# Kernel optimization log

Hardware: AMD Instinct MI355X
Metric: run time of the kernel (lower is better)

Reference implementation:

```python
import jax, jax.numpy as jnp
import numpy as np

B = 131072      # batch
IN = 1024       # input_dim
H = 384         # hidden[0]
L = 128         # latent_dim = hidden[1]
K = 32          # slots_k
R = 2           # top_r
TAU = 0.7


def setup_inputs() -> dict:
    key = jax.random.key(0)
    ks = jax.random.split(key, 8)
    s = 0.02
    f32 = jnp.float32
    return {
        "x":  jax.random.normal(ks[0], (B, IN), f32),
        "w1": jax.random.normal(ks[1], (IN, H), f32) * s,
        "b1": jnp.zeros((H,), f32),
        "w2": jax.random.normal(ks[2], (H, L), f32) * s,
        "b2": jnp.zeros((L,), f32),
        "mk": jax.random.normal(ks[3], (K, L), f32) * s,  # memory_keys
        "mv": jax.random.normal(ks[4], (K, L), f32) * s,  # memory_values
        "w3": jax.random.normal(ks[5], (2 * L, H), f32) * s,
        "b3": jnp.zeros((H,), f32),
        "w4": jax.random.normal(ks[6], (H, 1), f32) * s,
        "b4": jnp.zeros((1,), f32),
    }


def reference(x, w1, b1, w2, b2, mk, mv, w3, b3, w4, b4):
    # block_a: Linear -> GELU -> (Dropout=id in eval) -> Linear -> GELU
    z = jax.nn.gelu(x @ w1 + b1, approximate=False)
    z = jax.nn.gelu(z @ w2 + b2, approximate=False)          # [B, L]

    # top-r slot attention over memory bank
    logits = (z @ mk.T) / TAU                                 # [B, K]
    _, idx = jax.lax.top_k(logits, R)                         # [B, R]
    keep = jax.nn.one_hot(idx, K, dtype=logits.dtype).sum(-2) > 0  # [B, K] bool
    masked = jnp.where(keep, logits, -jnp.inf)
    attn = jax.nn.softmax(masked, axis=-1)                    # [B, K]
    mem = attn @ mv                                           # [B, L]

    fused = jnp.concatenate([z, mem], axis=-1)                # [B, 2L]

    # default head: Linear -> GELU -> Linear(.,1)
    h = jax.nn.gelu(fused @ w3 + b3, approximate=False)
    logit = (h @ w4 + b4)[..., 0]                             # [B]
    return jax.nn.sigmoid(logit)
```

## Files before the change

### kernel.cpp

```cpp
#include <hip/hip_runtime.h>

#define BATCH   131072
#define INDIM   1024
#define BM      64
#define BDIM    512
#define NBLK    (BATCH / BM)

#define WT_OFF   0
#define XT0_OFF  49152
#define XT1_OFF  57344
#define Z1_OFF   0
#define W2T0_OFF 50176
#define W2T1_OFF 58368
#define FZ_OFF   0
#define RP_OFF   33792
#define W3T_OFF  42240
#define CB_OFF   66816
#define B1S_OFF  (CB_OFF)
#define B2S_OFF  (CB_OFF + 1536)
#define B3S_OFF  (CB_OFF + 2048)
#define W4S_OFF  (CB_OFF + 3584)
#define MKS_OFF  (CB_OFF + 5120)
#define SMEM_BYTES (CB_OFF + 13824)

typedef unsigned short u16;
typedef u16    u16x8  __attribute__((ext_vector_type(8)));
typedef u16    u16x4  __attribute__((ext_vector_type(4)));
typedef __bf16 bf16x8 __attribute__((ext_vector_type(8)));
typedef __bf16 bf16x4 __attribute__((ext_vector_type(4)));
typedef float  f32x4  __attribute__((ext_vector_type(4)));

__device__ __forceinline__ u16 f2bf(float f) {
  unsigned u = __float_as_uint(f);
  u += 0x7FFFu + ((u >> 16) & 1u);
  return (u16)(u >> 16);
}

__device__ __forceinline__ float gelu_fast(float v) {
  float t = v * v;
  float u = v * fmaf(t, 0.0356774081f, 0.7978845608f);
  float e = __builtin_amdgcn_exp2f(u * -2.885390082f);
  return v * __builtin_amdgcn_rcpf(1.0f + e);
}

__device__ __forceinline__ f32x4 mfma16(u16x8 a, u16x8 b, f32x4 c) {
  return __builtin_amdgcn_mfma_f32_16x16x32_bf16(
      __builtin_bit_cast(bf16x8, a), __builtin_bit_cast(bf16x8, b), c, 0, 0, 0);
}

__device__ __forceinline__ u16x8 cvt8(float4 a, float4 b) {
  bf16x8 r;
  r[0]=(__bf16)a.x; r[1]=(__bf16)a.y; r[2]=(__bf16)a.z; r[3]=(__bf16)a.w;
  r[4]=(__bf16)b.x; r[5]=(__bf16)b.y; r[6]=(__bf16)b.z; r[7]=(__bf16)b.w;
  return __builtin_bit_cast(u16x8, r);
}
__device__ __forceinline__ u16x4 cvt4(float4 a) {
  bf16x4 r;
  r[0]=(__bf16)a.x; r[1]=(__bf16)a.y; r[2]=(__bf16)a.z; r[3]=(__bf16)a.w;
  return __builtin_bit_cast(u16x4, r);
}

typedef __attribute__((address_space(3))) unsigned int       lds_u32;
typedef __attribute__((address_space(1))) const unsigned int glb_u32;
__device__ __forceinline__ void gload16(const void* g, void* l) {
  __builtin_amdgcn_global_load_lds((glb_u32*)g, (lds_u32*)l, 16, 0, 0);
}

#define FENCE_SCHED __builtin_amdgcn_sched_barrier(0)
#define WAIT_LGKM0 do { asm volatile("s_waitcnt lgkmcnt(0)" ::: "memory"); FENCE_SCHED; } while (0)
#define WAIT_VMN(N) do { asm volatile("s_waitcnt vmcnt(" #N ")" ::: "memory"); FENCE_SCHED; } while (0)
#define BARRIER_LGKM do { \
  asm volatile("s_waitcnt lgkmcnt(0)" ::: "memory"); \
  __builtin_amdgcn_s_barrier(); FENCE_SCHED; } while (0)

__global__ void prep_kernel(const float* __restrict__ w1, const float* __restrict__ w2,
                            const float* __restrict__ w3, u16* __restrict__ w1s,
                            u16* __restrict__ w2s, u16* __restrict__ w3s) {
  int i = blockIdx.x * 256 + threadIdx.x;
  if (i < 393216) {
    int t = i / 24576, p = i % 24576;
    int r = p >> 6, q = p & 63, cp = q >> 3, o = q & 7;
    int k = t * 64 + ((cp ^ (r & 7)) << 3) + o;
    w1s[i] = f2bf(w1[k * 384 + r]);
  } else if (i < 442368) {
    int j = i - 393216;
    int t = j / 4096, p = j % 4096;
    int r = p >> 5, q = p & 31, cp = q >> 3, o = q & 7;
    int k = t * 32 + ((cp ^ ((r >> 1) & 3)) << 3) + o;
    w2s[j] = f2bf(w2[k * 128 + r]);
  } else if (i < 540672) {
    int j = i - 442368;
    int t = j / 12288, p = j % 12288;
    int r = p >> 5, q = p & 31, cp = q >> 3, o = q & 7;
    int k = t * 32 + ((cp ^ ((r >> 1) & 3)) << 3) + o;
    w3s[j] = f2bf(w3[k * 384 + r]);
  }
}

__global__ __launch_bounds__(BDIM, 4) void fused_kernel(
    const float* __restrict__ x,  const u16* __restrict__ w1s,
    const float* __restrict__ b1, const u16* __restrict__ w2s,
    const float* __restrict__ b2, const float* __restrict__ mkw,
    const float* __restrict__ mvw, const u16* __restrict__ w3s,
    const float* __restrict__ b3, const float* __restrict__ w4,
    const float* __restrict__ b4, float* __restrict__ out) {
  extern __shared__ char smem[];
  u16*   z1  = (u16*)(smem + Z1_OFF);
  u16*   fz  = (u16*)(smem + FZ_OFF);
  u16*   w3t = (u16*)(smem + W3T_OFF);
  float* b1s = (float*)(smem + B1S_OFF);
  float* b2s = (float*)(smem + B2S_OFF);
  float* b3s = (float*)(smem + B3S_OFF);
  float* w4s = (float*)(smem + W4S_OFF);
  u16*   mks = (u16*)(smem + MKS_OFF);
  float* rowpart = (float*)(smem + RP_OFF);

  const int tid  = threadIdx.x;
  const int lane = tid & 63;
  const int wid  = tid >> 6;
  const int l15  = lane & 15;
  const int g    = lane >> 4;
  const int swz8 = l15 & 7;
  const int swz4 = (l15 >> 1) & 3;
  const int row0 = blockIdx.x * BM;
  const int wrow = wid * 48;
  const int wstrip = wid * 3072;

  {
    const u16* ws = w1s + wstrip + lane * 8;
    u16* wd = (u16*)(smem + WT_OFF) + wstrip;
    #pragma unroll
    for (int i = 0; i < 6; ++i) gload16(ws + i * 512, wd + i * 512);
  }
  FENCE_SCHED;
  const int xrow = tid >> 3, xoct = tid & 7;
  const float* xp = x + (long)(row0 + xrow) * INDIM + xoct * 8;
  const int xdst = xrow * 64 + ((xoct ^ (xrow & 7)) << 3);
  float4 xa = *(const float4*)xp, xb = *(const float4*)(xp + 4);

  if (tid < 384) b1s[tid] = b1[tid];
  if (tid < 128) b2s[tid] = b2[tid];
  if (tid < 384) b3s[tid] = b3[tid];
  if (tid < 384) w4s[tid] = w4[tid];
  {
    int r = tid >> 4, cc = (tid & 15) * 8;
    const float4* p = (const float4*)(mkw + r * 128 + cc);
    *(u16x8*)(mks + r * 136 + cc) = cvt8(p[0], p[1]);
  }
  *(u16x8*)((u16*)(smem + XT0_OFF) + xdst) = cvt8(xa, xb);
  { const float* p = xp + 64; xa = *(const float4*)p; xb = *(const float4*)(p + 4); }
  BARRIER_LGKM;

  f32x4 acc[4][3];
  #pragma unroll
  for (int m = 0; m < 4; ++m)
    #pragma unroll
    for (int n = 0; n < 3; ++n) acc[m][n] = (f32x4){0.f, 0.f, 0.f, 0.f};

  const u16* wtb = (const u16*)(smem + WT_OFF);
  for (int kt = 0; kt < 16; ++kt) {
    if (kt < 15) { WAIT_VMN(2); } else { WAIT_VMN(0); }
    const u16* xtb = (const u16*)(smem + ((kt & 1) ? XT1_OFF : XT0_OFF));
    u16x8 af[4], bfr[3];
    const int c0 = (g ^ swz8) * 8;
    #pragma unroll
    for (int m = 0; m < 4; ++m) af[m] = *(const u16x8*)(xtb + (m * 16 + l15) * 64 + c0);
    #pragma unroll
    for (int n = 0; n < 3; ++n) bfr[n] = *(const u16x8*)(wtb + (wrow + n * 16 + l15) * 64 + c0);
    #pragma unroll
    for (int m = 0; m < 4; ++m)
      #pragma unroll
      for (int n = 0; n < 3; ++n) acc[m][n] = mfma16(bfr[n], af[m], acc[m][n]);
    const int c1 = ((g + 4) ^ swz8) * 8;
    #pragma unroll
    for (int m = 0; m < 4; ++m) af[m] = *(const u16x8*)(xtb + (m * 16 + l15) * 64 + c1);
    #pragma unroll
    for (int n = 0; n < 3; ++n) bfr[n] = *(const u16x8*)(wtb + (wrow + n * 16 + l15) * 64 + c1);
    WAIT_LGKM0;
    if (kt < 15) {
      const u16* ws = w1s + (kt + 1) * 24576 + wstrip + lane * 8;
      u16* wd = (u16*)(smem + WT_OFF) + wstrip;
      #pragma unroll
      for (int i = 0; i < 6; ++i) gload16(ws + i * 512, wd + i * 512);
      FENCE_SCHED;
      u16* xn = (u16*)(smem + ((kt & 1) ? XT0_OFF : XT1_OFF));
      *(u16x8*)(xn + xdst) = cvt8(xa, xb);
      if (kt < 14) {
        const float* p = xp + (kt + 2) * 64;
        xa = *(const float4*)p; xb = *(const float4*)(p + 4);
      }
      BARRIER_LGKM;
    }
    #pragma unroll
    for (int m = 0; m < 4; ++m)
      #pragma unroll
      for (int n = 0; n < 3; ++n) acc[m][n] = mfma16(bfr[n], af[m], acc[m][n]);
  }
  BARRIER_LGKM;

  {
    const u16* s2 = w2s + wid * 512 + lane * 8;
    gload16(s2, (u16*)(smem + W2T0_OFF) + wid * 512);
    const u16* s2b = w2s + 4096 + wid * 512 + lane * 8;
    gload16(s2b, (u16*)(smem + W2T1_OFF) + wid * 512);
  }
  #pragma unroll
  for (int m = 0; m < 4; ++m) {
    #pragma unroll
    for (int n = 0; n < 3; ++n) {
      int col = wrow + n * 16 + g * 4;
      float4 bv = *(const float4*)(b1s + col);
      f32x4 a = acc[m][n];
      float4 gv = {gelu_fast(a[0] + bv.x), gelu_fast(a[1] + bv.y),
                   gelu_fast(a[2] + bv.z), gelu_fast(a[3] + bv.w)};
      *(u16x4*)(z1 + (m * 16 + l15) * 392 + col) = cvt4(gv);
    }
  }
  BARRIER_LGKM;

  f32x4 acc2[4];
  #pragma unroll
  for (int m = 0; m < 4; ++m) acc2[m] = (f32x4){0.f, 0.f, 0.f, 0.f};
  for (int kt = 0; kt < 12; ++kt) {
    if (kt < 10) { WAIT_VMN(1); } else { WAIT_VMN(0); }
    const u16* wb = (const u16*)(smem + ((kt & 1) ? W2T1_OFF : W2T0_OFF));
    u16x8 a2f[4];
    #pragma unroll
    for (int m = 0; m < 4; ++m)
      a2f[m] = *(const u16x8*)(z1 + (m * 16 + l15) * 392 + kt * 32 + g * 8);
    u16x8 b2f = *(const u16x8*)(wb + (wid * 16 + l15) * 32 + (g ^ swz4) * 8);
    WAIT_LGKM0;
    if (kt < 10) {
      const u16* s2 = w2s + (kt + 2) * 4096 + wid * 512 + lane * 8;
      gload16(s2, (u16*)(smem + ((kt & 1) ? W2T1_OFF : W2T0_OFF)) + wid * 512);
    }
    #pragma unroll
    for (int m = 0; m < 4; ++m) acc2[m] = mfma16(b2f, a2f[m], acc2[m]);
  }
  BARRIER_LGKM;

  {
    const u16* s3 = w3s + wid * 1536 + lane * 8;
    u16* d3 = w3t + wid * 1536;
    gload16(s3, d3); gload16(s3 + 512, d3 + 512); gload16(s3 + 1024, d3 + 1024);
  }
  #pragma unroll
  for (int m = 0; m < 4; ++m) {
    int col = wid * 16 + g * 4;
    float4 bv = *(const float4*)(b2s + col);
    f32x4 a = acc2[m];
    float4 gv = {gelu_fast(a[0] + bv.x), gelu_fast(a[1] + bv.y),
                 gelu_fast(a[2] + bv.z), gelu_fast(a[3] + bv.w)};
    *(u16x4*)(fz + (m * 16 + l15) * 264 + col) = cvt4(gv);
  }
  BARRIER_LGKM;

  if (wid < 4) {
    const int wr = wid * 16 + l15;
    f32x4 accl[2] = {(f32x4){0,0,0,0}, (f32x4){0,0,0,0}};
    #pragma unroll
    for (int ks = 0; ks < 4; ++ks) {
      u16x8 afz = *(const u16x8*)(fz + wr * 264 + ks * 32 + g * 8);
      u16x8 k0  = *(const u16x8*)(mks + l15 * 136 + ks * 32 + g * 8);
      u16x8 k1  = *(const u16x8*)(mks + (16 + l15) * 136 + ks * 32 + g * 8);
      accl[0] = mfma16(k0, afz, accl[0]);
      accl[1] = mfma16(k1, afz, accl[1]);
    }
    float m1 = -3.4e38f, m2 = -3.4e38f; int i1 = -1, i2 = -1;
    #pragma unroll
    for (int n = 0; n < 2; ++n)
      #pragma unroll
      for (int j = 0; j < 4; ++j) {
        float v = accl[n][j]; int idx = n * 16 + g * 4 + j;
        if (v > m1) { m2 = m1; i2 = i1; m1 = v; i1 = idx; }
        else if (v > m2) { m2 = v; i2 = idx; }
      }
    #pragma unroll
    for (int d = 16; d <= 32; d <<= 1) {
      float om1 = __shfl_xor(m1, d); int oi1 = __shfl_xor(i1, d);
      float om2 = __shfl_xor(m2, d); int oi2 = __shfl_xor(i2, d);
      bool take = (om1 > m1) || (om1 == m1 && oi1 < i1);
      if (take) {
        float nm2; int ni2;
        if (m1 > om2 || (m1 == om2 && i1 < oi2)) { nm2 = m1; ni2 = i1; }
        else { nm2 = om2; ni2 = oi2; }
        m1 = om1; i1 = oi1; m2 = nm2; i2 = ni2;
      } else {
        if (om1 > m2 || (om1 == m2 && oi1 < i2)) { m2 = om1; i2 = oi1; }
      }
    }
    float a1 = __builtin_amdgcn_rcpf(
        1.0f + __builtin_amdgcn_exp2f((m2 - m1) * (1.44269504f / 0.7f)));
    float a2 = 1.0f - a1;
    const float* v1 = mvw + i1 * 128 + g * 32;
    const float* v2 = mvw + i2 * 128 + g * 32;
    #pragma unroll
    for (int c = 0; c < 4; ++c) {
      float4 A0 = *(const float4*)(v1 + c * 8), A1 = *(const float4*)(v1 + c * 8 + 4);
      float4 B0 = *(const float4*)(v2 + c * 8), B1 = *(const float4*)(v2 + c * 8 + 4);
      float4 r0 = {a1*A0.x + a2*B0.x, a1*A0.y + a2*B0.y, a1*A0.z + a2*B0.z, a1*A0.w + a2*B0.w};
      float4 r1 = {a1*A1.x + a2*B1.x, a1*A1.y + a2*B1.y, a1*A1.z + a2*B1.z, a1*A1.w + a2*B1.w};
      *(u16x8*)(fz + wr * 264 + 128 + g * 32 + c * 8) = cvt8(r0, r1);
    }
  }
  BARRIER_LGKM;

  f32x4 acc3[4][3];
  #pragma unroll
  for (int m = 0; m < 4; ++m)
    #pragma unroll
    for (int n = 0; n < 3; ++n) acc3[m][n] = (f32x4){0.f, 0.f, 0.f, 0.f};
  for (int kt = 0; kt < 8; ++kt) {
    WAIT_VMN(0);
    u16x8 a3f[4], b3f[3];
    #pragma unroll
    for (int m = 0; m < 4; ++m)
      a3f[m] = *(const u16x8*)(fz + (m * 16 + l15) * 264 + kt * 32 + g * 8);
    #pragma unroll
    for (int n = 0; n < 3; ++n)
      b3f[n] = *(const u16x8*)(w3t + (wrow + n * 16 + l15) * 32 + (g ^ swz4) * 8);
    WAIT_LGKM0;
    if (kt < 7) {
      const u16* s3 = w3s + (kt + 1) * 12288 + wid * 1536 + lane * 8;
      u16* d3 = w3t + wid * 1536;
      gload16(s3, d3); gload16(s3 + 512, d3 + 512); gload16(s3 + 1024, d3 + 1024);
    }
    #pragma unroll
    for (int m = 0; m < 4; ++m)
      #pragma unroll
      for (int n = 0; n < 3; ++n) acc3[m][n] = mfma16(b3f[n], a3f[m], acc3[m][n]);
  }

  #pragma unroll
  for (int m = 0; m < 4; ++m) {
    float s = 0.f;
    #pragma unroll
    for (int n = 0; n < 3; ++n) {
      int col = wrow + n * 16 + g * 4;
      float4 bv = *(const float4*)(b3s + col);
      float4 wv = *(const float4*)(w4s + col);
      f32x4 a = acc3[m][n];
      s += gelu_fast(a[0] + bv.x) * wv.x + gelu_fast(a[1] + bv.y) * wv.y +
           gelu_fast(a[2] + bv.z) * wv.z + gelu_fast(a[3] + bv.w) * wv.w;
    }
    s += __shfl_xor(s, 16);
    s += __shfl_xor(s, 32);
    if (lane < 16) rowpart[(m * 16 + l15) * 8 + wid] = s;
  }
  BARRIER_LGKM;
  if (tid < BM) {
    const float4* rp = (const float4*)(rowpart + tid * 8);
    float4 p0 = rp[0], p1 = rp[1];
    float lg = b4[0] + p0.x + p0.y + p0.z + p0.w + p1.x + p1.y + p1.z + p1.w;
    out[row0 + tid] = __builtin_amdgcn_rcpf(1.0f + __builtin_amdgcn_exp2f(-lg * 1.44269504f));
  }
}

extern "C" void kernel_launch(void* const* d_in, const int* in_sizes, int n_in,
                              void* d_out, int out_size, void* d_ws, size_t ws_size,
                              hipStream_t stream) {
  const float* x  = (const float*)d_in[0];
  const float* w1 = (const float*)d_in[1];
  const float* b1 = (const float*)d_in[2];
  const float* w2 = (const float*)d_in[3];
  const float* b2 = (const float*)d_in[4];
  const float* mk = (const float*)d_in[5];
  const float* mv = (const float*)d_in[6];
  const float* w3 = (const float*)d_in[7];
  const float* b3 = (const float*)d_in[8];
  const float* w4 = (const float*)d_in[9];
  const float* b4 = (const float*)d_in[10];

  u16* w1s = (u16*)d_ws;
  u16* w2s = w1s + 393216;
  u16* w3s = w1s + 442368;

  prep_kernel<<<2112, 256, 0, stream>>>(w1, w2, w3, w1s, w2s, w3s);

  (void)hipFuncSetAttribute(reinterpret_cast<const void*>(fused_kernel),
                            hipFuncAttributeMaxDynamicSharedMemorySize, SMEM_BYTES);
  fused_kernel<<<NBLK, BDIM, SMEM_BYTES, stream>>>(x, w1s, b1, w2s, b2, mk, mv, w3s,
                                                   b3, w4, b4, (float*)d_out);
}
```

Baseline: 232.0 us.

## Double-buffer W1 tiles with k=32 sub-tiles to overlap loads with MFMA

Restructures the first GEMM's K loop from a single 64-wide W1 buffer, refilled after all its fragments were read, into two 32-wide W1 buffers (wt0/wt1). Each half-tile's refill is issued right after its fragments are read, so global-to-LDS loads overlap MFMA work on the other buffer. X staging is split into two 32-wide halves per step, with one barrier per 64 of K and an explicit prologue and epilogue. The prep kernel re-swizzles W1 to the k=32 layout, and the swizzle index is unified across stages. It adds code size and register pressure and relies on exact vmcnt bookkeeping.

```diff
diff --git a/kernel.cpp b/kernel.cpp
--- a/kernel.cpp
+++ b/kernel.cpp
@@ -6,9 +6,10 @@
 #define BDIM    512
 #define NBLK    (BATCH / BM)
 
-#define WT_OFF   0
-#define XT0_OFF  49152
-#define XT1_OFF  57344
+#define WT0_OFF  0
+#define WT1_OFF  24576
+#define XTA_OFF  49152
+#define XTB_OFF  57344
 #define Z1_OFF   0
 #define W2T0_OFF 50176
 #define W2T1_OFF 58368
@@ -78,9 +79,9 @@
                             u16* __restrict__ w2s, u16* __restrict__ w3s) {
   int i = blockIdx.x * 256 + threadIdx.x;
   if (i < 393216) {
-    int t = i / 24576, p = i % 24576;
-    int r = p >> 6, q = p & 63, cp = q >> 3, o = q & 7;
-    int k = t * 64 + ((cp ^ (r & 7)) << 3) + o;
+    int t = i / 12288, p = i % 12288;
+    int r = p >> 5, q = p & 31, cp = q >> 3, o = q & 7;
+    int k = t * 32 + ((cp ^ ((r >> 1) & 3)) << 3) + o;
     w1s[i] = f2bf(w1[k * 384 + r]);
   } else if (i < 442368) {
     int j = i - 393216;
@@ -108,6 +109,8 @@
   u16*   z1  = (u16*)(smem + Z1_OFF);
   u16*   fz  = (u16*)(smem + FZ_OFF);
   u16*   w3t = (u16*)(smem + W3T_OFF);
+  u16*   wt0 = (u16*)(smem + WT0_OFF);
+  u16*   wt1 = (u16*)(smem + WT1_OFF);
   float* b1s = (float*)(smem + B1S_OFF);
   float* b2s = (float*)(smem + B2S_OFF);
   float* b3s = (float*)(smem + B3S_OFF);
@@ -120,23 +123,10 @@
   const int wid  = tid >> 6;
   const int l15  = lane & 15;
   const int g    = lane >> 4;
-  const int swz8 = l15 & 7;
-  const int swz4 = (l15 >> 1) & 3;
+  const int sw8  = (g ^ ((l15 >> 1) & 3)) * 8;
   const int row0 = blockIdx.x * BM;
   const int wrow = wid * 48;
-  const int wstrip = wid * 3072;
-
-  {
-    const u16* ws = w1s + wstrip + lane * 8;
-    u16* wd = (u16*)(smem + WT_OFF) + wstrip;
-    #pragma unroll
-    for (int i = 0; i < 6; ++i) gload16(ws + i * 512, wd + i * 512);
-  }
-  FENCE_SCHED;
-  const int xrow = tid >> 3, xoct = tid & 7;
-  const float* xp = x + (long)(row0 + xrow) * INDIM + xoct * 8;
-  const int xdst = xrow * 64 + ((xoct ^ (xrow & 7)) << 3);
-  float4 xa = *(const float4*)xp, xb = *(const float4*)(xp + 4);
+  const int wstrip = wid * 1536;
 
   if (tid < 384) b1s[tid] = b1[tid];
   if (tid < 128) b2s[tid] = b2[tid];
@@ -147,8 +137,22 @@
     const float4* p = (const float4*)(mkw + r * 128 + cc);
     *(u16x8*)(mks + r * 136 + cc) = cvt8(p[0], p[1]);
   }
-  *(u16x8*)((u16*)(smem + XT0_OFF) + xdst) = cvt8(xa, xb);
-  { const float* p = xp + 64; xa = *(const float4*)p; xb = *(const float4*)(p + 4); }
+  {
+    const u16* ws = w1s + wstrip + lane * 8;
+    gload16(ws, wt0 + wstrip); gload16(ws + 512, wt0 + wstrip + 512);
+    gload16(ws + 1024, wt0 + wstrip + 1024);
+    const u16* ws1 = ws + 12288;
+    gload16(ws1, wt1 + wstrip); gload16(ws1 + 512, wt1 + wstrip + 512);
+    gload16(ws1 + 1024, wt1 + wstrip + 1024);
+  }
+  FENCE_SCHED;
+  const int xrow = tid >> 3, xq = tid & 7;
+  const float* xp = x + (long)(row0 + xrow) * INDIM + xq * 4;
+  const int xpub = xrow * 32 + (((xq >> 1) ^ ((xrow >> 1) & 3)) << 3) + (xq & 1) * 4;
+  float4 xA = *(const float4*)xp, xB = *(const float4*)(xp + 32);
+  *(u16x4*)((u16*)(smem + XTA_OFF) + xpub)        = cvt4(xA);
+  *(u16x4*)((u16*)(smem + XTA_OFF) + 2048 + xpub) = cvt4(xB);
+  xA = *(const float4*)(xp + 64); xB = *(const float4*)(xp + 96);
   BARRIER_LGKM;
 
   f32x4 acc[4][3];
@@ -157,44 +161,114 @@
     #pragma unroll
     for (int n = 0; n < 3; ++n) acc[m][n] = (f32x4){0.f, 0.f, 0.f, 0.f};
 
-  const u16* wtb = (const u16*)(smem + WT_OFF);
-  for (int kt = 0; kt < 16; ++kt) {
-    if (kt < 15) { WAIT_VMN(2); } else { WAIT_VMN(0); }
-    const u16* xtb = (const u16*)(smem + ((kt & 1) ? XT1_OFF : XT0_OFF));
-    u16x8 af[4], bfr[3];
-    const int c0 = (g ^ swz8) * 8;
-    #pragma unroll
-    for (int m = 0; m < 4; ++m) af[m] = *(const u16x8*)(xtb + (m * 16 + l15) * 64 + c0);
-    #pragma unroll
-    for (int n = 0; n < 3; ++n) bfr[n] = *(const u16x8*)(wtb + (wrow + n * 16 + l15) * 64 + c0);
-    #pragma unroll
-    for (int m = 0; m < 4; ++m)
-      #pragma unroll
-      for (int n = 0; n < 3; ++n) acc[m][n] = mfma16(bfr[n], af[m], acc[m][n]);
-    const int c1 = ((g + 4) ^ swz8) * 8;
-    #pragma unroll
-    for (int m = 0; m < 4; ++m) af[m] = *(const u16x8*)(xtb + (m * 16 + l15) * 64 + c1);
-    #pragma unroll
-    for (int n = 0; n < 3; ++n) bfr[n] = *(const u16x8*)(wtb + (wrow + n * 16 + l15) * 64 + c1);
-    WAIT_LGKM0;
-    if (kt < 15) {
-      const u16* ws = w1s + (kt + 1) * 24576 + wstrip + lane * 8;
-      u16* wd = (u16*)(smem + WT_OFF) + wstrip;
-      #pragma unroll
-      for (int i = 0; i < 6; ++i) gload16(ws + i * 512, wd + i * 512);
-      FENCE_SCHED;
-      u16* xn = (u16*)(smem + ((kt & 1) ? XT0_OFF : XT1_OFF));
-      *(u16x8*)(xn + xdst) = cvt8(xa, xb);
-      if (kt < 14) {
-        const float* p = xp + (kt + 2) * 64;
-        xa = *(const float4*)p; xb = *(const float4*)(p + 4);
-      }
-      BARRIER_LGKM;
-    }
-    #pragma unroll
-    for (int m = 0; m < 4; ++m)
-      #pragma unroll
-      for (int n = 0; n < 3; ++n) acc[m][n] = mfma16(bfr[n], af[m], acc[m][n]);
+  for (int p = 0; p < 14; ++p) {
+    const u16* xrb = (const u16*)(smem + ((p & 1) ? XTB_OFF : XTA_OFF));
+    u16* xwb = (u16*)(smem + ((p & 1) ? XTA_OFF : XTB_OFF));
+    WAIT_VMN(5);
+    {
+      u16x8 af[4], bfr[3];
+      #pragma unroll
+      for (int m = 0; m < 4; ++m) af[m] = *(const u16x8*)(xrb + (m * 16 + l15) * 32 + sw8);
+      #pragma unroll
+      for (int n = 0; n < 3; ++n) bfr[n] = *(const u16x8*)(wt0 + (wrow + n * 16 + l15) * 32 + sw8);
+      WAIT_LGKM0;
+      const u16* ws = w1s + (2 * p + 2) * 12288 + wstrip + lane * 8;
+      gload16(ws, wt0 + wstrip); gload16(ws + 512, wt0 + wstrip + 512);
+      gload16(ws + 1024, wt0 + wstrip + 1024);
+      #pragma unroll
+      for (int m = 0; m < 4; ++m)
+        #pragma unroll
+        for (int n = 0; n < 3; ++n) acc[m][n] = mfma16(bfr[n], af[m], acc[m][n]);
+    }
+    WAIT_VMN(5);
+    {
+      u16x8 af[4], bfr[3];
+      #pragma unroll
+      for (int m = 0; m < 4; ++m) af[m] = *(const u16x8*)(xrb + 2048 + (m * 16 + l15) * 32 + sw8);
+      #pragma unroll
+      for (int n = 0; n < 3; ++n) bfr[n] = *(const u16x8*)(wt1 + (wrow + n * 16 + l15) * 32 + sw8);
+      WAIT_LGKM0;
+      const u16* ws = w1s + (2 * p + 3) * 12288 + wstrip + lane * 8;
+      gload16(ws, wt1 + wstrip); gload16(ws + 512, wt1 + wstrip + 512);
+      gload16(ws + 1024, wt1 + wstrip + 1024);
+      #pragma unroll
+      for (int m = 0; m < 4; ++m)
+        #pragma unroll
+        for (int n = 0; n < 3; ++n) acc[m][n] = mfma16(bfr[n], af[m], acc[m][n]);
+    }
+    *(u16x4*)(xwb + xpub)        = cvt4(xA);
+    *(u16x4*)(xwb + 2048 + xpub) = cvt4(xB);
+    xA = *(const float4*)(xp + (2 * p + 4) * 32);
+    xB = *(const float4*)(xp + (2 * p + 5) * 32);
+    BARRIER_LGKM;
+  }
+  {
+    const u16* xrb = (const u16*)(smem + XTA_OFF);
+    u16* xwb = (u16*)(smem + XTB_OFF);
+    WAIT_VMN(5);
+    {
+      u16x8 af[4], bfr[3];
+      #pragma unroll
+      for (int m = 0; m < 4; ++m) af[m] = *(const u16x8*)(xrb + (m * 16 + l15) * 32 + sw8);
+      #pragma unroll
+      for (int n = 0; n < 3; ++n) bfr[n] = *(const u16x8*)(wt0 + (wrow + n * 16 + l15) * 32 + sw8);
+      WAIT_LGKM0;
+      const u16* ws = w1s + 30 * 12288 + wstrip + lane * 8;
+      gload16(ws, wt0 + wstrip); gload16(ws + 512, wt0 + wstrip + 512);
+      gload16(ws + 1024, wt0 + wstrip + 1024);
+      #pragma unroll
+      for (int m = 0; m < 4; ++m)
+        #pragma unroll
+        for (int n = 0; n < 3; ++n) acc[m][n] = mfma16(bfr[n], af[m], acc[m][n]);
+    }
+    WAIT_VMN(5);
+    {
+      u16x8 af[4], bfr[3];
+      #pragma unroll
+      for (int m = 0; m < 4; ++m) af[m] = *(const u16x8*)(xrb + 2048 + (m * 16 + l15) * 32 + sw8);
+      #pragma unroll
+      for (int n = 0; n < 3; ++n) bfr[n] = *(const u16x8*)(wt1 + (wrow + n * 16 + l15) * 32 + sw8);
+      WAIT_LGKM0;
+      const u16* ws = w1s + 31 * 12288 + wstrip + lane * 8;
+      gload16(ws, wt1 + wstrip); gload16(ws + 512, wt1 + wstrip + 512);
+      gload16(ws + 1024, wt1 + wstrip + 1024);
+      #pragma unroll
+      for (int m = 0; m < 4; ++m)
+        #pragma unroll
+        for (int n = 0; n < 3; ++n) acc[m][n] = mfma16(bfr[n], af[m], acc[m][n]);
+    }
+    *(u16x4*)(xwb + xpub)        = cvt4(xA);
+    *(u16x4*)(xwb + 2048 + xpub) = cvt4(xB);
+    BARRIER_LGKM;
+  }
+  {
+    const u16* xrb = (const u16*)(smem + XTB_OFF);
+    WAIT_VMN(3);
+    {
+      u16x8 af[4], bfr[3];
+      #pragma unroll
+      for (int m = 0; m < 4; ++m) af[m] = *(const u16x8*)(xrb + (m * 16 + l15) * 32 + sw8);
+      #pragma unroll
+      for (int n = 0; n < 3; ++n) bfr[n] = *(const u16x8*)(wt0 + (wrow + n * 16 + l15) * 32 + sw8);
+      WAIT_LGKM0;
+      #pragma unroll
+      for (int m = 0; m < 4; ++m)
+        #pragma unroll
+        for (int n = 0; n < 3; ++n) acc[m][n] = mfma16(bfr[n], af[m], acc[m][n]);
+    }
+    WAIT_VMN(0);
+    {
+      u16x8 af[4], bfr[3];
+      #pragma unroll
+      for (int m = 0; m < 4; ++m) af[m] = *(const u16x8*)(xrb + 2048 + (m * 16 + l15) * 32 + sw8);
+      #pragma unroll
+      for (int n = 0; n < 3; ++n) bfr[n] = *(const u16x8*)(wt1 + (wrow + n * 16 + l15) * 32 + sw8);
+      WAIT_LGKM0;
+      #pragma unroll
+      for (int m = 0; m < 4; ++m)
+        #pragma unroll
+        for (int n = 0; n < 3; ++n) acc[m][n] = mfma16(bfr[n], af[m], acc[m][n]);
+    }
   }
   BARRIER_LGKM;
 
@@ -228,7 +302,7 @@
     #pragma unroll
     for (int m = 0; m < 4; ++m)
       a2f[m] = *(const u16x8*)(z1 + (m * 16 + l15) * 392 + kt * 32 + g * 8);
-    u16x8 b2f = *(const u16x8*)(wb + (wid * 16 + l15) * 32 + (g ^ swz4) * 8);
+    u16x8 b2f = *(const u16x8*)(wb + (wid * 16 + l15) * 32 + sw8);
     WAIT_LGKM0;
     if (kt < 10) {
       const u16* s2 = w2s + (kt + 2) * 4096 + wid * 512 + lane * 8;
@@ -318,7 +392,7 @@
       a3f[m] = *(const u16x8*)(fz + (m * 16 + l15) * 264 + kt * 32 + g * 8);
     #pragma unroll
     for (int n = 0; n < 3; ++n)
-      b3f[n] = *(const u16x8*)(w3t + (wrow + n * 16 + l15) * 32 + (g ^ swz4) * 8);
+      b3f[n] = *(const u16x8*)(w3t + (wrow + n * 16 + l15) * 32 + sw8);
     WAIT_LGKM0;
     if (kt < 7) {
       const u16* s3 = w3s + (kt + 1) * 12288 + wid * 1536 + lane * 8;
```

After: 229.0 us. No clear change (-1.3%).

## Load weights directly into registers in MFMA fragment layout instead of staging via LDS

Applied to the files above, without the earlier changes.

The prep kernel now lays out W1, W2 and W3 in per-lane MFMA fragment order, so each wave reads its weight fragments straight from global/L2 into registers with register double-buffering. The LDS weight staging (global_load_lds, swizzles, vmcnt waits) is removed, leaving LDS for the x tiles and the activations. The x tile is restructured into two 32-wide K halves per barrier step, which halves the number of block barriers in the first GEMM. Launch bounds drop to 2 blocks per CU, which gives more registers but lowers occupancy, and every block now re-reads the weights from L2 with no reuse in LDS.

```diff
diff --git a/kernel.cpp b/kernel.cpp
--- a/kernel.cpp
+++ b/kernel.cpp
@@ -6,16 +6,12 @@
 #define BDIM    512
 #define NBLK    (BATCH / BM)
 
-#define WT_OFF   0
-#define XT0_OFF  49152
-#define XT1_OFF  57344
 #define Z1_OFF   0
-#define W2T0_OFF 50176
-#define W2T1_OFF 58368
 #define FZ_OFF   0
 #define RP_OFF   33792
-#define W3T_OFF  42240
-#define CB_OFF   66816
+#define XTA_OFF  50176
+#define XTB_OFF  58368
+#define CB_OFF   66560
 #define B1S_OFF  (CB_OFF)
 #define B2S_OFF  (CB_OFF + 1536)
 #define B3S_OFF  (CB_OFF + 2048)
@@ -60,54 +56,53 @@
   return __builtin_bit_cast(u16x4, r);
 }
 
-typedef __attribute__((address_space(3))) unsigned int       lds_u32;
-typedef __attribute__((address_space(1))) const unsigned int glb_u32;
-__device__ __forceinline__ void gload16(const void* g, void* l) {
-  __builtin_amdgcn_global_load_lds((glb_u32*)g, (lds_u32*)l, 16, 0, 0);
-}
-
-#define FENCE_SCHED __builtin_amdgcn_sched_barrier(0)
-#define WAIT_LGKM0 do { asm volatile("s_waitcnt lgkmcnt(0)" ::: "memory"); FENCE_SCHED; } while (0)
-#define WAIT_VMN(N) do { asm volatile("s_waitcnt vmcnt(" #N ")" ::: "memory"); FENCE_SCHED; } while (0)
 #define BARRIER_LGKM do { \
   asm volatile("s_waitcnt lgkmcnt(0)" ::: "memory"); \
-  __builtin_amdgcn_s_barrier(); FENCE_SCHED; } while (0)
+  __builtin_amdgcn_s_barrier(); \
+  __builtin_amdgcn_sched_barrier(0); } while (0)
 
 __global__ void prep_kernel(const float* __restrict__ w1, const float* __restrict__ w2,
-                            const float* __restrict__ w3, u16* __restrict__ w1s,
-                            u16* __restrict__ w2s, u16* __restrict__ w3s) {
+                            const float* __restrict__ w3, u16* __restrict__ w1f,
+                            u16* __restrict__ w2f, u16* __restrict__ w3f) {
   int i = blockIdx.x * 256 + threadIdx.x;
   if (i < 393216) {
-    int t = i / 24576, p = i % 24576;
-    int r = p >> 6, q = p & 63, cp = q >> 3, o = q & 7;
-    int k = t * 64 + ((cp ^ (r & 7)) << 3) + o;
-    w1s[i] = f2bf(w1[k * 384 + r]);
+    int o = i & 7, lane = (i >> 3) & 63;
+    int rest = i >> 9;
+    int n = rest % 3, rw = rest / 3;
+    int wid = rw & 7, kt = rw >> 3;
+    int col = wid * 48 + n * 16 + (lane & 15);
+    int k = kt * 32 + (lane >> 4) * 8 + o;
+    w1f[i] = f2bf(w1[k * 384 + col]);
   } else if (i < 442368) {
     int j = i - 393216;
-    int t = j / 4096, p = j % 4096;
-    int r = p >> 5, q = p & 31, cp = q >> 3, o = q & 7;
-    int k = t * 32 + ((cp ^ ((r >> 1) & 3)) << 3) + o;
-    w2s[j] = f2bf(w2[k * 128 + r]);
+    int o = j & 7, lane = (j >> 3) & 63;
+    int rest = j >> 9;
+    int wid = rest & 7, kt = rest >> 3;
+    int col = wid * 16 + (lane & 15);
+    int k = kt * 32 + (lane >> 4) * 8 + o;
+    w2f[j] = f2bf(w2[k * 128 + col]);
   } else if (i < 540672) {
     int j = i - 442368;
-    int t = j / 12288, p = j % 12288;
-    int r = p >> 5, q = p & 31, cp = q >> 3, o = q & 7;
-    int k = t * 32 + ((cp ^ ((r >> 1) & 3)) << 3) + o;
-    w3s[j] = f2bf(w3[k * 384 + r]);
-  }
-}
-
-__global__ __launch_bounds__(BDIM, 4) void fused_kernel(
-    const float* __restrict__ x,  const u16* __restrict__ w1s,
-    const float* __restrict__ b1, const u16* __restrict__ w2s,
+    int o = j & 7, lane = (j >> 3) & 63;
+    int rest = j >> 9;
+    int n = rest % 3, rw = rest / 3;
+    int wid = rw & 7, kt = rw >> 3;
+    int col = wid * 48 + n * 16 + (lane & 15);
+    int k = kt * 32 + (lane >> 4) * 8 + o;
+    w3f[j] = f2bf(w3[k * 384 + col]);
+  }
+}
+
+__global__ __launch_bounds__(BDIM, 2) void fused_kernel(
+    const float* __restrict__ x,  const u16* __restrict__ w1f,
+    const float* __restrict__ b1, const u16* __restrict__ w2f,
     const float* __restrict__ b2, const float* __restrict__ mkw,
-    const float* __restrict__ mvw, const u16* __restrict__ w3s,
+    const float* __restrict__ mvw, const u16* __restrict__ w3f,
     const float* __restrict__ b3, const float* __restrict__ w4,
     const float* __restrict__ b4, float* __restrict__ out) {
   extern __shared__ char smem[];
   u16*   z1  = (u16*)(smem + Z1_OFF);
   u16*   fz  = (u16*)(smem + FZ_OFF);
-  u16*   w3t = (u16*)(smem + W3T_OFF);
   float* b1s = (float*)(smem + B1S_OFF);
   float* b2s = (float*)(smem + B2S_OFF);
   float* b3s = (float*)(smem + B3S_OFF);
@@ -120,23 +115,22 @@
   const int wid  = tid >> 6;
   const int l15  = lane & 15;
   const int g    = lane >> 4;
-  const int swz8 = l15 & 7;
-  const int swz4 = (l15 >> 1) & 3;
+  const int sw8  = (g ^ ((l15 >> 1) & 3)) * 8;
   const int row0 = blockIdx.x * BM;
   const int wrow = wid * 48;
-  const int wstrip = wid * 3072;
-
-  {
-    const u16* ws = w1s + wstrip + lane * 8;
-    u16* wd = (u16*)(smem + WT_OFF) + wstrip;
-    #pragma unroll
-    for (int i = 0; i < 6; ++i) gload16(ws + i * 512, wd + i * 512);
-  }
-  FENCE_SCHED;
-  const int xrow = tid >> 3, xoct = tid & 7;
-  const float* xp = x + (long)(row0 + xrow) * INDIM + xoct * 8;
-  const int xdst = xrow * 64 + ((xoct ^ (xrow & 7)) << 3);
-  float4 xa = *(const float4*)xp, xb = *(const float4*)(xp + 4);
+
+  const u16* wp1 = w1f + wid * 1536 + lane * 8;
+  u16x8 wf0[3], wf1[3];
+  #pragma unroll
+  for (int n = 0; n < 3; ++n) wf0[n] = *(const u16x8*)(wp1 + n * 512);
+  #pragma unroll
+  for (int n = 0; n < 3; ++n) wf1[n] = *(const u16x8*)(wp1 + 12288 + n * 512);
+
+  const int xrow = tid >> 3, xq = tid & 7;
+  const float* xp = x + (long)(row0 + xrow) * INDIM + xq * 4;
+  const int xpub = xrow * 32 + (((xq >> 1) ^ ((xrow >> 1) & 3)) << 3) + (xq & 1) * 4;
+  float4 xA = *(const float4*)xp;
+  float4 xB = *(const float4*)(xp + 32);
 
   if (tid < 384) b1s[tid] = b1[tid];
   if (tid < 128) b2s[tid] = b2[tid];
@@ -144,11 +138,12 @@
   if (tid < 384) w4s[tid] = w4[tid];
   {
     int r = tid >> 4, cc = (tid & 15) * 8;
-    const float4* p = (const float4*)(mkw + r * 128 + cc);
-    *(u16x8*)(mks + r * 136 + cc) = cvt8(p[0], p[1]);
-  }
-  *(u16x8*)((u16*)(smem + XT0_OFF) + xdst) = cvt8(xa, xb);
-  { const float* p = xp + 64; xa = *(const float4*)p; xb = *(const float4*)(p + 4); }
+    const float4* pm = (const float4*)(mkw + r * 128 + cc);
+    *(u16x8*)(mks + r * 136 + cc) = cvt8(pm[0], pm[1]);
+  }
+  *(u16x4*)((u16*)(smem + XTA_OFF) + xpub)        = cvt4(xA);
+  *(u16x4*)((u16*)(smem + XTA_OFF) + 2048 + xpub) = cvt4(xB);
+  xA = *(const float4*)(xp + 64); xB = *(const float4*)(xp + 96);
   BARRIER_LGKM;
 
   f32x4 acc[4][3];
@@ -157,52 +152,52 @@
     #pragma unroll
     for (int n = 0; n < 3; ++n) acc[m][n] = (f32x4){0.f, 0.f, 0.f, 0.f};
 
-  const u16* wtb = (const u16*)(smem + WT_OFF);
-  for (int kt = 0; kt < 16; ++kt) {
-    if (kt < 15) { WAIT_VMN(2); } else { WAIT_VMN(0); }
-    const u16* xtb = (const u16*)(smem + ((kt & 1) ? XT1_OFF : XT0_OFF));
-    u16x8 af[4], bfr[3];
-    const int c0 = (g ^ swz8) * 8;
-    #pragma unroll
-    for (int m = 0; m < 4; ++m) af[m] = *(const u16x8*)(xtb + (m * 16 + l15) * 64 + c0);
-    #pragma unroll
-    for (int n = 0; n < 3; ++n) bfr[n] = *(const u16x8*)(wtb + (wrow + n * 16 + l15) * 64 + c0);
-    #pragma unroll
-    for (int m = 0; m < 4; ++m)
-      #pragma unroll
-      for (int n = 0; n < 3; ++n) acc[m][n] = mfma16(bfr[n], af[m], acc[m][n]);
-    const int c1 = ((g + 4) ^ swz8) * 8;
-    #pragma unroll
-    for (int m = 0; m < 4; ++m) af[m] = *(const u16x8*)(xtb + (m * 16 + l15) * 64 + c1);
-    #pragma unroll
-    for (int n = 0; n < 3; ++n) bfr[n] = *(const u16x8*)(wtb + (wrow + n * 16 + l15) * 64 + c1);
-    WAIT_LGKM0;
-    if (kt < 15) {
-      const u16* ws = w1s + (kt + 1) * 24576 + wstrip + lane * 8;
-      u16* wd = (u16*)(smem + WT_OFF) + wstrip;
-      #pragma unroll
-      for (int i = 0; i < 6; ++i) gload16(ws + i * 512, wd + i * 512);
-      FENCE_SCHED;
-      u16* xn = (u16*)(smem + ((kt & 1) ? XT0_OFF : XT1_OFF));
-      *(u16x8*)(xn + xdst) = cvt8(xa, xb);
-      if (kt < 14) {
-        const float* p = xp + (kt + 2) * 64;
-        xa = *(const float4*)p; xb = *(const float4*)(p + 4);
-      }
-      BARRIER_LGKM;
-    }
-    #pragma unroll
-    for (int m = 0; m < 4; ++m)
-      #pragma unroll
-      for (int n = 0; n < 3; ++n) acc[m][n] = mfma16(bfr[n], af[m], acc[m][n]);
-  }
-  BARRIER_LGKM;
-
+  for (int p = 0; p < 15; ++p) {
+    const u16* xrb = (const u16*)(smem + ((p & 1) ? XTB_OFF : XTA_OFF));
+    u16* xwb = (u16*)(smem + ((p & 1) ? XTA_OFF : XTB_OFF));
+    u16x8 af0[4], af1[4];
+    #pragma unroll
+    for (int m = 0; m < 4; ++m) af0[m] = *(const u16x8*)(xrb + (m * 16 + l15) * 32 + sw8);
+    #pragma unroll
+    for (int m = 0; m < 4; ++m) af1[m] = *(const u16x8*)(xrb + 2048 + (m * 16 + l15) * 32 + sw8);
+    u16x8 wn0[3], wn1[3];
+    #pragma unroll
+    for (int n = 0; n < 3; ++n) wn0[n] = *(const u16x8*)(wp1 + (2 * p + 2) * 12288 + n * 512);
+    #pragma unroll
+    for (int n = 0; n < 3; ++n) wn1[n] = *(const u16x8*)(wp1 + (2 * p + 3) * 12288 + n * 512);
+    #pragma unroll
+    for (int m = 0; m < 4; ++m)
+      #pragma unroll
+      for (int n = 0; n < 3; ++n) acc[m][n] = mfma16(wf0[n], af0[m], acc[m][n]);
+    *(u16x4*)(xwb + xpub)        = cvt4(xA);
+    *(u16x4*)(xwb + 2048 + xpub) = cvt4(xB);
+    if (p < 14) {
+      xA = *(const float4*)(xp + (2 * p + 4) * 32);
+      xB = *(const float4*)(xp + (2 * p + 5) * 32);
+    }
+    #pragma unroll
+    for (int m = 0; m < 4; ++m)
+      #pragma unroll
+      for (int n = 0; n < 3; ++n) acc[m][n] = mfma16(wf1[n], af1[m], acc[m][n]);
+    #pragma unroll
+    for (int n = 0; n < 3; ++n) { wf0[n] = wn0[n]; wf1[n] = wn1[n]; }
+    BARRIER_LGKM;
+  }
   {
-    const u16* s2 = w2s + wid * 512 + lane * 8;
-    gload16(s2, (u16*)(smem + W2T0_OFF) + wid * 512);
-    const u16* s2b = w2s + 4096 + wid * 512 + lane * 8;
-    gload16(s2b, (u16*)(smem + W2T1_OFF) + wid * 512);
+    const u16* xrb = (const u16*)(smem + XTB_OFF);
+    u16x8 af0[4], af1[4];
+    #pragma unroll
+    for (int m = 0; m < 4; ++m) af0[m] = *(const u16x8*)(xrb + (m * 16 + l15) * 32 + sw8);
+    #pragma unroll
+    for (int m = 0; m < 4; ++m) af1[m] = *(const u16x8*)(xrb + 2048 + (m * 16 + l15) * 32 + sw8);
+    #pragma unroll
+    for (int m = 0; m < 4; ++m)
+      #pragma unroll
+      for (int n = 0; n < 3; ++n) acc[m][n] = mfma16(wf0[n], af0[m], acc[m][n]);
+    #pragma unroll
+    for (int m = 0; m < 4; ++m)
+      #pragma unroll
+      for (int n = 0; n < 3; ++n) acc[m][n] = mfma16(wf1[n], af1[m], acc[m][n]);
   }
   #pragma unroll
   for (int m = 0; m < 4; ++m) {
@@ -218,32 +213,23 @@
   }
   BARRIER_LGKM;
 
+  const u16* wp2 = w2f + wid * 512 + lane * 8;
   f32x4 acc2[4];
   #pragma unroll
   for (int m = 0; m < 4; ++m) acc2[m] = (f32x4){0.f, 0.f, 0.f, 0.f};
+  u16x8 w2c = *(const u16x8*)wp2;
   for (int kt = 0; kt < 12; ++kt) {
-    if (kt < 10) { WAIT_VMN(1); } else { WAIT_VMN(0); }
-    const u16* wb = (const u16*)(smem + ((kt & 1) ? W2T1_OFF : W2T0_OFF));
     u16x8 a2f[4];
     #pragma unroll
     for (int m = 0; m < 4; ++m)
       a2f[m] = *(const u16x8*)(z1 + (m * 16 + l15) * 392 + kt * 32 + g * 8);
-    u16x8 b2f = *(const u16x8*)(wb + (wid * 16 + l15) * 32 + (g ^ swz4) * 8);
-    WAIT_LGKM0;
-    if (kt < 10) {
-      const u16* s2 = w2s + (kt + 2) * 4096 + wid * 512 + lane * 8;
-      gload16(s2, (u16*)(smem + ((kt & 1) ? W2T1_OFF : W2T0_OFF)) + wid * 512);
-    }
-    #pragma unroll
-    for (int m = 0; m < 4; ++m) acc2[m] = mfma16(b2f, a2f[m], acc2[m]);
-  }
-  BARRIER_LGKM;
-
-  {
-    const u16* s3 = w3s + wid * 1536 + lane * 8;
-    u16* d3 = w3t + wid * 1536;
-    gload16(s3, d3); gload16(s3 + 512, d3 + 512); gload16(s3 + 1024, d3 + 1024);
-  }
+    u16x8 w2n = (kt < 11) ? *(const u16x8*)(wp2 + (kt + 1) * 4096) : w2c;
+    #pragma unroll
+    for (int m = 0; m < 4; ++m) acc2[m] = mfma16(w2c, a2f[m], acc2[m]);
+    w2c = w2n;
+  }
+  BARRIER_LGKM;
+
   #pragma unroll
   for (int m = 0; m < 4; ++m) {
     int col = wid * 16 + g * 4;
@@ -305,30 +291,29 @@
   }
   BARRIER_LGKM;
 
+  const u16* wp3 = w3f + wid * 1536 + lane * 8;
   f32x4 acc3[4][3];
   #pragma unroll
   for (int m = 0; m < 4; ++m)
     #pragma unroll
     for (int n = 0; n < 3; ++n) acc3[m][n] = (f32x4){0.f, 0.f, 0.f, 0.f};
+  u16x8 w3c[3];
+  #pragma unroll
+  for (int n = 0; n < 3; ++n) w3c[n] = *(const u16x8*)(wp3 + n * 512);
   for (int kt = 0; kt < 8; ++kt) {
-    WAIT_VMN(0);
-    u16x8 a3f[4], b3f[3];
+    u16x8 a3f[4], w3n[3];
     #pragma unroll
     for (int m = 0; m < 4; ++m)
       a3f[m] = *(const u16x8*)(fz + (m * 16 + l15) * 264 + kt * 32 + g * 8);
     #pragma unroll
     for (int n = 0; n < 3; ++n)
-      b3f[n] = *(const u16x8*)(w3t + (wrow + n * 16 + l15) * 32 + (g ^ swz4) * 8);
-    WAIT_LGKM0;
-    if (kt < 7) {
-      const u16* s3 = w3s + (kt + 1) * 12288 + wid * 1536 + lane * 8;
-      u16* d3 = w3t + wid * 1536;
-      gload16(s3, d3); gload16(s3 + 512, d3 + 512); gload16(s3 + 1024, d3 + 1024);
-    }
-    #pragma unroll
-    for (int m = 0; m < 4; ++m)
-      #pragma unroll
-      for (int n = 0; n < 3; ++n) acc3[m][n] = mfma16(b3f[n], a3f[m], acc3[m][n]);
+      w3n[n] = (kt < 7) ? *(const u16x8*)(wp3 + (kt + 1) * 12288 + n * 512) : w3c[n];
+    #pragma unroll
+    for (int m = 0; m < 4; ++m)
+      #pragma unroll
+      for (int n = 0; n < 3; ++n) acc3[m][n] = mfma16(w3c[n], a3f[m], acc3[m][n]);
+    #pragma unroll
+    for (int n = 0; n < 3; ++n) w3c[n] = w3n[n];
   }
 
   #pragma unroll
@@ -371,14 +356,14 @@
   const float* w4 = (const float*)d_in[9];
   const float* b4 = (const float*)d_in[10];
 
-  u16* w1s = (u16*)d_ws;
-  u16* w2s = w1s + 393216;
-  u16* w3s = w1s + 442368;
-
-  prep_kernel<<<2112, 256, 0, stream>>>(w1, w2, w3, w1s, w2s, w3s);
+  u16* w1f = (u16*)d_ws;
+  u16* w2f = w1f + 393216;
+  u16* w3f = w1f + 442368;
+
+  prep_kernel<<<2112, 256, 0, stream>>>(w1, w2, w3, w1f, w2f, w3f);
 
   (void)hipFuncSetAttribute(reinterpret_cast<const void*>(fused_kernel),
                             hipFuncAttributeMaxDynamicSharedMemorySize, SMEM_BYTES);
-  fused_kernel<<<NBLK, BDIM, SMEM_BYTES, stream>>>(x, w1s, b1, w2s, b2, mk, mv, w3s,
+  fused_kernel<<<NBLK, BDIM, SMEM_BYTES, stream>>>(x, w1f, b1, w2f, b2, mk, mv, w3f,
                                                    b3, w4, b4, (float*)d_out);
 }
```

Measured after the change: 271.8 us. +17.2%, slower.

## Double-buffer W1 tiles with K=32 steps and register-prefetched fragments in GEMM1

Applied to the files above, without the earlier changes.

Restructures the first GEMM's main loop from 16 steps of K=64 with a single W1 buffer into 32 steps of K=32. W1 and X each get two LDS buffers, the W1 prep layout and swizzle change to match, and the next step's fragments are loaded into registers while the current MFMAs run. MFMA sections are wrapped in s_setprio in GEMM1 and GEMM3. Launch bounds drop from 4 to 2 blocks per SM, which loosens register pressure but may lower occupancy, and the loop now takes twice as many barriers.

```diff
diff --git a/kernel.cpp b/kernel.cpp
--- a/kernel.cpp
+++ b/kernel.cpp
@@ -6,9 +6,10 @@
 #define BDIM    512
 #define NBLK    (BATCH / BM)
 
-#define WT_OFF   0
+#define WT0_OFF  0
+#define WT1_OFF  24576
 #define XT0_OFF  49152
-#define XT1_OFF  57344
+#define XT1_OFF  53248
 #define Z1_OFF   0
 #define W2T0_OFF 50176
 #define W2T1_OFF 58368
@@ -69,6 +70,7 @@
 #define FENCE_SCHED __builtin_amdgcn_sched_barrier(0)
 #define WAIT_LGKM0 do { asm volatile("s_waitcnt lgkmcnt(0)" ::: "memory"); FENCE_SCHED; } while (0)
 #define WAIT_VMN(N) do { asm volatile("s_waitcnt vmcnt(" #N ")" ::: "memory"); FENCE_SCHED; } while (0)
+#define SOFT_VM0 asm volatile("s_waitcnt vmcnt(0)" ::: "memory")
 #define BARRIER_LGKM do { \
   asm volatile("s_waitcnt lgkmcnt(0)" ::: "memory"); \
   __builtin_amdgcn_s_barrier(); FENCE_SCHED; } while (0)
@@ -78,9 +80,9 @@
                             u16* __restrict__ w2s, u16* __restrict__ w3s) {
   int i = blockIdx.x * 256 + threadIdx.x;
   if (i < 393216) {
-    int t = i / 24576, p = i % 24576;
-    int r = p >> 6, q = p & 63, cp = q >> 3, o = q & 7;
-    int k = t * 64 + ((cp ^ (r & 7)) << 3) + o;
+    int t = i / 12288, p = i % 12288;
+    int r = p >> 5, q = p & 31, cp = q >> 3, o = q & 7;
+    int k = t * 32 + ((cp ^ ((r >> 1) & 3)) << 3) + o;
     w1s[i] = f2bf(w1[k * 384 + r]);
   } else if (i < 442368) {
     int j = i - 393216;
@@ -97,7 +99,7 @@
   }
 }
 
-__global__ __launch_bounds__(BDIM, 4) void fused_kernel(
+__global__ __launch_bounds__(BDIM, 2) void fused_kernel(
     const float* __restrict__ x,  const u16* __restrict__ w1s,
     const float* __restrict__ b1, const u16* __restrict__ w2s,
     const float* __restrict__ b2, const float* __restrict__ mkw,
@@ -108,6 +110,8 @@
   u16*   z1  = (u16*)(smem + Z1_OFF);
   u16*   fz  = (u16*)(smem + FZ_OFF);
   u16*   w3t = (u16*)(smem + W3T_OFF);
+  u16*   wt0 = (u16*)(smem + WT0_OFF);
+  u16*   wt1 = (u16*)(smem + WT1_OFF);
   float* b1s = (float*)(smem + B1S_OFF);
   float* b2s = (float*)(smem + B2S_OFF);
   float* b3s = (float*)(smem + B3S_OFF);
@@ -120,23 +124,10 @@
   const int wid  = tid >> 6;
   const int l15  = lane & 15;
   const int g    = lane >> 4;
-  const int swz8 = l15 & 7;
-  const int swz4 = (l15 >> 1) & 3;
+  const int sw8  = (g ^ ((l15 >> 1) & 3)) * 8;
   const int row0 = blockIdx.x * BM;
   const int wrow = wid * 48;
-  const int wstrip = wid * 3072;
-
-  {
-    const u16* ws = w1s + wstrip + lane * 8;
-    u16* wd = (u16*)(smem + WT_OFF) + wstrip;
-    #pragma unroll
-    for (int i = 0; i < 6; ++i) gload16(ws + i * 512, wd + i * 512);
-  }
-  FENCE_SCHED;
-  const int xrow = tid >> 3, xoct = tid & 7;
-  const float* xp = x + (long)(row0 + xrow) * INDIM + xoct * 8;
-  const int xdst = xrow * 64 + ((xoct ^ (xrow & 7)) << 3);
-  float4 xa = *(const float4*)xp, xb = *(const float4*)(xp + 4);
+  const int wstrip = wid * 1536;
 
   if (tid < 384) b1s[tid] = b1[tid];
   if (tid < 128) b2s[tid] = b2[tid];
@@ -144,11 +135,26 @@
   if (tid < 384) w4s[tid] = w4[tid];
   {
     int r = tid >> 4, cc = (tid & 15) * 8;
-    const float4* p = (const float4*)(mkw + r * 128 + cc);
-    *(u16x8*)(mks + r * 136 + cc) = cvt8(p[0], p[1]);
-  }
-  *(u16x8*)((u16*)(smem + XT0_OFF) + xdst) = cvt8(xa, xb);
-  { const float* p = xp + 64; xa = *(const float4*)p; xb = *(const float4*)(p + 4); }
+    const float4* pm = (const float4*)(mkw + r * 128 + cc);
+    *(u16x8*)(mks + r * 136 + cc) = cvt8(pm[0], pm[1]);
+  }
+  {
+    const u16* ws = w1s + wstrip + lane * 8;
+    gload16(ws, wt0 + wstrip); gload16(ws + 512, wt0 + wstrip + 512);
+    gload16(ws + 1024, wt0 + wstrip + 1024);
+    const u16* ws1 = ws + 12288;
+    gload16(ws1, wt1 + wstrip); gload16(ws1 + 512, wt1 + wstrip + 512);
+    gload16(ws1 + 1024, wt1 + wstrip + 1024);
+  }
+  FENCE_SCHED;
+  const int xrow = tid >> 3, xq = tid & 7;
+  const float* xp = x + (long)(row0 + xrow) * INDIM + xq * 4;
+  const int xpub = xrow * 32 + (((xq >> 1) ^ ((xrow >> 1) & 3)) << 3) + (xq & 1) * 4;
+  float4 xP = *(const float4*)xp;
+  *(u16x4*)((u16*)(smem + XT0_OFF) + xpub) = cvt4(xP);
+  xP = *(const float4*)(xp + 32);
+  *(u16x4*)((u16*)(smem + XT1_OFF) + xpub) = cvt4(xP);
+  xP = *(const float4*)(xp + 64);
   BARRIER_LGKM;
 
   f32x4 acc[4][3];
@@ -157,46 +163,55 @@
     #pragma unroll
     for (int n = 0; n < 3; ++n) acc[m][n] = (f32x4){0.f, 0.f, 0.f, 0.f};
 
-  const u16* wtb = (const u16*)(smem + WT_OFF);
-  for (int kt = 0; kt < 16; ++kt) {
-    if (kt < 15) { WAIT_VMN(2); } else { WAIT_VMN(0); }
-    const u16* xtb = (const u16*)(smem + ((kt & 1) ? XT1_OFF : XT0_OFF));
-    u16x8 af[4], bfr[3];
-    const int c0 = (g ^ swz8) * 8;
-    #pragma unroll
-    for (int m = 0; m < 4; ++m) af[m] = *(const u16x8*)(xtb + (m * 16 + l15) * 64 + c0);
-    #pragma unroll
-    for (int n = 0; n < 3; ++n) bfr[n] = *(const u16x8*)(wtb + (wrow + n * 16 + l15) * 64 + c0);
+  u16x8 Aa[4], Ba[3], Ab[4], Bb[3];
+  #pragma unroll
+  for (int m = 0; m < 4; ++m)
+    Aa[m] = *(const u16x8*)((const u16*)(smem + XT0_OFF) + (m * 16 + l15) * 32 + sw8);
+  #pragma unroll
+  for (int n = 0; n < 3; ++n)
+    Ba[n] = *(const u16x8*)(wt0 + (wrow + n * 16 + l15) * 32 + sw8);
+
+#define G1_PHASE(KT, AC, BC, AN, BN)                                            \
+  do {                                                                          \
+    SOFT_VM0;       \
+    const u16* xnb = (const u16*)(smem + ((((KT) + 1) & 1) ? XT1_OFF : XT0_OFF)); \
+    const u16* wnb = (((KT) + 1) & 1) ? wt1 : wt0;                              \
+    _Pragma("unroll")                                                           \
+    for (int m = 0; m < 4; ++m)                                                 \
+      AN[m] = *(const u16x8*)(xnb + (m * 16 + l15) * 32 + sw8);                 \
+    _Pragma("unroll")                                                           \
+    for (int n = 0; n < 3; ++n)                                                 \
+      BN[n] = *(const u16x8*)(wnb + (wrow + n * 16 + l15) * 32 + sw8);          \
+    if ((KT) < 30) {   \
+      const u16* ws = w1s + ((KT) + 2) * 12288 + wstrip + lane * 8;             \
+      u16* wd = ((((KT) & 1)) ? wt1 : wt0) + wstrip;                            \
+      gload16(ws, wd); gload16(ws + 512, wd + 512); gload16(ws + 1024, wd + 1024); \
+    }                                                                           \
+    __builtin_amdgcn_s_setprio(1);                                              \
+    _Pragma("unroll")                                                           \
+    for (int m = 0; m < 4; ++m)                                                 \
+      _Pragma("unroll")                                                         \
+      for (int n = 0; n < 3; ++n) acc[m][n] = mfma16(BC[n], AC[m], acc[m][n]);  \
+    __builtin_amdgcn_s_setprio(0);                                              \
+    if ((KT) < 30) {                       \
+      u16* xw = (u16*)(smem + ((((KT) & 1)) ? XT1_OFF : XT0_OFF));              \
+      *(u16x4*)(xw + xpub) = cvt4(xP);                                          \
+      if ((KT) < 29) xP = *(const float4*)(xp + ((KT) + 3) * 32);               \
+    }                                                                           \
+    BARRIER_LGKM;                                                               \
+  } while (0)
+
+  for (int p = 0; p < 15; ++p) {
+    G1_PHASE(2 * p,     Aa, Ba, Ab, Bb);
+    G1_PHASE(2 * p + 1, Ab, Bb, Aa, Ba);
+  }
+  G1_PHASE(30, Aa, Ba, Ab, Bb);
+  {
     #pragma unroll
     for (int m = 0; m < 4; ++m)
       #pragma unroll
-      for (int n = 0; n < 3; ++n) acc[m][n] = mfma16(bfr[n], af[m], acc[m][n]);
-    const int c1 = ((g + 4) ^ swz8) * 8;
-    #pragma unroll
-    for (int m = 0; m < 4; ++m) af[m] = *(const u16x8*)(xtb + (m * 16 + l15) * 64 + c1);
-    #pragma unroll
-    for (int n = 0; n < 3; ++n) bfr[n] = *(const u16x8*)(wtb + (wrow + n * 16 + l15) * 64 + c1);
-    WAIT_LGKM0;
-    if (kt < 15) {
-      const u16* ws = w1s + (kt + 1) * 24576 + wstrip + lane * 8;
-      u16* wd = (u16*)(smem + WT_OFF) + wstrip;
-      #pragma unroll
-      for (int i = 0; i < 6; ++i) gload16(ws + i * 512, wd + i * 512);
-      FENCE_SCHED;
-      u16* xn = (u16*)(smem + ((kt & 1) ? XT0_OFF : XT1_OFF));
-      *(u16x8*)(xn + xdst) = cvt8(xa, xb);
-      if (kt < 14) {
-        const float* p = xp + (kt + 2) * 64;
-        xa = *(const float4*)p; xb = *(const float4*)(p + 4);
-      }
-      BARRIER_LGKM;
-    }
-    #pragma unroll
-    for (int m = 0; m < 4; ++m)
-      #pragma unroll
-      for (int n = 0; n < 3; ++n) acc[m][n] = mfma16(bfr[n], af[m], acc[m][n]);
-  }
-  BARRIER_LGKM;
+      for (int n = 0; n < 3; ++n) acc[m][n] = mfma16(Bb[n], Ab[m], acc[m][n]);
+  }
 
   {
     const u16* s2 = w2s + wid * 512 + lane * 8;
@@ -228,7 +243,7 @@
     #pragma unroll
     for (int m = 0; m < 4; ++m)
       a2f[m] = *(const u16x8*)(z1 + (m * 16 + l15) * 392 + kt * 32 + g * 8);
-    u16x8 b2f = *(const u16x8*)(wb + (wid * 16 + l15) * 32 + (g ^ swz4) * 8);
+    u16x8 b2f = *(const u16x8*)(wb + (wid * 16 + l15) * 32 + sw8);
     WAIT_LGKM0;
     if (kt < 10) {
       const u16* s2 = w2s + (kt + 2) * 4096 + wid * 512 + lane * 8;
@@ -318,17 +333,19 @@
       a3f[m] = *(const u16x8*)(fz + (m * 16 + l15) * 264 + kt * 32 + g * 8);
     #pragma unroll
     for (int n = 0; n < 3; ++n)
-      b3f[n] = *(const u16x8*)(w3t + (wrow + n * 16 + l15) * 32 + (g ^ swz4) * 8);
+      b3f[n] = *(const u16x8*)(w3t + (wrow + n * 16 + l15) * 32 + sw8);
     WAIT_LGKM0;
     if (kt < 7) {
       const u16* s3 = w3s + (kt + 1) * 12288 + wid * 1536 + lane * 8;
       u16* d3 = w3t + wid * 1536;
       gload16(s3, d3); gload16(s3 + 512, d3 + 512); gload16(s3 + 1024, d3 + 1024);
     }
+    __builtin_amdgcn_s_setprio(1);
     #pragma unroll
     for (int m = 0; m < 4; ++m)
       #pragma unroll
       for (int n = 0; n < 3; ++n) acc3[m][n] = mfma16(b3f[n], a3f[m], acc3[m][n]);
+    __builtin_amdgcn_s_setprio(0);
   }
 
   #pragma unroll
```

New measurement: 352.3 us. 1.52x slower.
